# Performance work log

Measured on AMD Instinct MI355X. Metric: run time of the kernel, lower is better.

The kernel has to match this reference:

```python
import jax, jax.numpy as jnp
import numpy as np


def setup_inputs() -> dict:
    key = jax.random.key(0)
    ks = jax.random.split(key, 8)
    B, N, C, H = 4, 1024, 512, 8
    return {
        "x": jax.random.normal(ks[0], (B, N, C), jnp.float32),
        "pos": jax.random.normal(ks[1], (B, N, 3), jnp.float32),
        "w_qkv": jax.random.normal(ks[2], (C, 3 * C), jnp.float32) * 0.02,
        "b_qkv": jax.random.normal(ks[3], (3 * C,), jnp.float32) * 0.02,
        "w1": jax.random.normal(ks[4], (3, 64), jnp.float32) * 0.1,
        "b1": jax.random.normal(ks[5], (64,), jnp.float32) * 0.1,
        "w2": jax.random.normal(ks[6], (64, H), jnp.float32) * 0.1,
        "b2": jax.random.normal(ks[7], (H,), jnp.float32) * 0.1,
    }


def reference(x, pos, w_qkv, b_qkv, w1, b1, w2, b2):
    B, N, C = x.shape
    H = w2.shape[1]          # num_heads
    D = C // H               # head_dim
    scale = D ** (-0.5)

    # qkv projection -> q, k, v each [B, H, N, D]
    qkv = (x @ w_qkv + b_qkv).reshape(B, N, 3, H, D)
    qkv = jnp.transpose(qkv, (2, 0, 3, 1, 4))
    q, k, v = qkv[0], qkv[1], qkv[2]

    # pairwise unit direction vectors [B, N, N, 3]
    pos_diff = pos[:, :, None, :] - pos[:, None, :, :]
    pos_norm = jnp.linalg.norm(pos_diff, axis=-1, keepdims=True) + 1e-6
    pos_dir = pos_diff / pos_norm

    # position-MLP bias: [B, N, N, H] -> [B, H, N, N]
    h = jax.nn.relu(pos_dir @ w1 + b1)
    bias = jnp.transpose(h @ w2 + b2, (0, 3, 1, 2))

    attn = jnp.einsum("bhnd,bhmd->bhnm", q, k) * scale + bias
    attn = jax.nn.softmax(attn, axis=-1)
    out = jnp.einsum("bhnm,bhmd->bhnd", attn, v)
    return jnp.transpose(out, (0, 2, 1, 3)).reshape(B, N, C)
```

## Files before the change

kernel.cpp:

```cpp
#include <hip/hip_runtime.h>
#include <hip/hip_bf16.h>
#include <hip/hip_fp16.h>
#include <math.h>


typedef __attribute__((ext_vector_type(8))) short bh8;
typedef __attribute__((ext_vector_type(4))) float f32x4;

#define LOG2E 1.44269504f

static __device__ __forceinline__ ushort f2bf(float x) {
    __hip_bfloat16 h = __float2bfloat16(x);
    return *reinterpret_cast<ushort*>(&h);
}
static __device__ __forceinline__ float bf2f(ushort u) {
    unsigned v = ((unsigned)u) << 16;
    return __builtin_bit_cast(float, v);
}
static __device__ __forceinline__ ushort f2h(float x) {
    __half h = __float2half(x);
    return *reinterpret_cast<ushort*>(&h);
}
static __device__ __forceinline__ float h2f(ushort u) {
    __half h = __builtin_bit_cast(__half, u);
    return __half2float(h);
}

__global__ __launch_bounds__(256) void prep_kernel(
    const float* __restrict__ x, const float* __restrict__ pos,
    const float* __restrict__ w1, const float* __restrict__ wqkv,
    ushort* __restrict__ xh, ushort* __restrict__ xl,
    ushort* __restrict__ wTh, ushort* __restrict__ wTl,
    float* __restrict__ apos)
{
    __shared__ float t[64][65];
    const int bid = blockIdx.x;
    const int tid = threadIdx.x;

    if (bid < 2048) {
        const int idx = bid * 256 + tid;
        const float4 v = *(const float4*)&x[(size_t)idx * 4];
        ushort h0 = f2bf(v.x), h1 = f2bf(v.y), h2 = f2bf(v.z), h3 = f2bf(v.w);
        ushort l0 = f2bf(v.x - bf2f(h0)), l1 = f2bf(v.y - bf2f(h1));
        ushort l2 = f2bf(v.z - bf2f(h2)), l3 = f2bf(v.w - bf2f(h3));
        uint2 hu, lu;
        hu.x = (unsigned)h0 | ((unsigned)h1 << 16);
        hu.y = (unsigned)h2 | ((unsigned)h3 << 16);
        lu.x = (unsigned)l0 | ((unsigned)l1 << 16);
        lu.y = (unsigned)l2 | ((unsigned)l3 << 16);
        *(uint2*)&xh[(size_t)idx * 4] = hu;
        *(uint2*)&xl[(size_t)idx * 4] = lu;
    } else if (bid < 3072) {
        const int idx = (bid - 2048) * 256 + tid;
        const int bn = idx >> 6, j = idx & 63;
        const float px = pos[bn * 3 + 0];
        const float py = pos[bn * 3 + 1];
        const float pz = pos[bn * 3 + 2];
        apos[idx] = fmaf(px, w1[j], fmaf(py, w1[64 + j], pz * w1[128 + j]));
    } else {
        const int tb = bid - 3072;
        const int n0 = (tb % 24) * 64;
        const int k0 = (tb / 24) * 64;
        const int c = tid & 63, r4 = tid >> 6;
#pragma unroll
        for (int i = 0; i < 16; ++i) {
            const int r = i * 4 + r4;
            t[r][c] = wqkv[(size_t)(k0 + r) * 1536 + n0 + c];
        }
        __syncthreads();
#pragma unroll
        for (int i = 0; i < 16; ++i) {
            const int r = i * 4 + r4;
            const float v = t[c][r];
            const ushort hv = f2bf(v);
            wTh[(size_t)(n0 + r) * 512 + k0 + c] = hv;
            wTl[(size_t)(n0 + r) * 512 + k0 + c] = f2bf(v - bf2f(hv));
        }
    }
}

__global__ __launch_bounds__(256, 2) void qkv_mfma(
    const ushort* __restrict__ xh, const ushort* __restrict__ xl,
    const ushort* __restrict__ wTh, const ushort* __restrict__ wTl,
    const float* __restrict__ bqkv,
    ushort* __restrict__ qb, ushort* __restrict__ kb, ushort* __restrict__ vTb)
{
    __shared__ ushort Ah[128 * 68], Al[128 * 68], Bh[128 * 68], Bl[128 * 68];
    const int tid = threadIdx.x;
    const int m0 = blockIdx.x * 128;
    const int n0 = blockIdx.y * 128;
    const int wid = tid >> 6, lane = tid & 63;
    const int wr = wid >> 1, wc = wid & 1;
    const int lq = lane & 15, g = lane >> 4;

    f32x4 acc[4][4];
#pragma unroll
    for (int m = 0; m < 4; ++m)
#pragma unroll
        for (int n = 0; n < 4; ++n) acc[m][n] = (f32x4){0.f, 0.f, 0.f, 0.f};

    const int srow = tid >> 3;
    const int sc8 = (tid & 7) * 8;

    for (int kt = 0; kt < 8; ++kt) {
        const int kk0 = kt * 64;
        __syncthreads();
#pragma unroll
        for (int i = 0; i < 4; ++i) {
            const int row = i * 32 + srow;
            *(bh8*)&Ah[row * 68 + sc8] =
                *(const bh8*)&xh[(size_t)(m0 + row) * 512 + kk0 + sc8];
            *(bh8*)&Al[row * 68 + sc8] =
                *(const bh8*)&xl[(size_t)(m0 + row) * 512 + kk0 + sc8];
            *(bh8*)&Bh[row * 68 + sc8] =
                *(const bh8*)&wTh[(size_t)(n0 + row) * 512 + kk0 + sc8];
            *(bh8*)&Bl[row * 68 + sc8] =
                *(const bh8*)&wTl[(size_t)(n0 + row) * 512 + kk0 + sc8];
        }
        __syncthreads();
#pragma unroll
        for (int kc = 0; kc < 2; ++kc) {
            const int ko = kc * 32 + g * 8;
            bh8 afh[4], afl[4], bfh[4], bfl[4];
#pragma unroll
            for (int m = 0; m < 4; ++m) {
                afh[m] = *(const bh8*)&Ah[(wr * 64 + m * 16 + lq) * 68 + ko];
                afl[m] = *(const bh8*)&Al[(wr * 64 + m * 16 + lq) * 68 + ko];
            }
#pragma unroll
            for (int n = 0; n < 4; ++n) {
                bfh[n] = *(const bh8*)&Bh[(wc * 64 + n * 16 + lq) * 68 + ko];
                bfl[n] = *(const bh8*)&Bl[(wc * 64 + n * 16 + lq) * 68 + ko];
            }
#pragma unroll
            for (int m = 0; m < 4; ++m)
#pragma unroll
                for (int n = 0; n < 4; ++n) {
                    acc[m][n] = __builtin_amdgcn_mfma_f32_16x16x32_bf16(
                        afh[m], bfh[n], acc[m][n], 0, 0, 0);
                    acc[m][n] = __builtin_amdgcn_mfma_f32_16x16x32_bf16(
                        afh[m], bfl[n], acc[m][n], 0, 0, 0);
                    acc[m][n] = __builtin_amdgcn_mfma_f32_16x16x32_bf16(
                        afl[m], bfh[n], acc[m][n], 0, 0, 0);
                }
        }
    }

    const int s = n0 >> 9;
    const int rowB = m0 + wr * 64;
    const int b = rowB >> 10;
    const float QSCALE = 0.125f * LOG2E;
#pragma unroll
    for (int nt = 0; nt < 4; ++nt) {
        const int col = n0 + wc * 64 + nt * 16 + lq;
        const float bias_v = bqkv[col];
        const int h = (col >> 6) & 7, d = col & 63;
#pragma unroll
        for (int mt = 0; mt < 4; ++mt) {
            const int nloc = (rowB & 1023) + mt * 16 + g * 4;
            const float v0 = acc[mt][nt][0] + bias_v;
            const float v1 = acc[mt][nt][1] + bias_v;
            const float v2 = acc[mt][nt][2] + bias_v;
            const float v3 = acc[mt][nt][3] + bias_v;
            if (s == 0) {
                const size_t base = ((size_t)(b * 8 + h) * 1024 + nloc) * 64 + d;
                qb[base]       = f2bf(v0 * QSCALE);
                qb[base + 64]  = f2bf(v1 * QSCALE);
                qb[base + 128] = f2bf(v2 * QSCALE);
                qb[base + 192] = f2bf(v3 * QSCALE);
            } else if (s == 1) {
                const size_t base = ((size_t)(b * 8 + h) * 1024 + nloc) * 64 + d;
                kb[base]       = f2bf(v0);
                kb[base + 64]  = f2bf(v1);
                kb[base + 128] = f2bf(v2);
                kb[base + 192] = f2bf(v3);
            } else {
                uint2 u;
                u.x = (unsigned)f2bf(v0) | ((unsigned)f2bf(v1) << 16);
                u.y = (unsigned)f2bf(v2) | ((unsigned)f2bf(v3) << 16);
                *(uint2*)&vTb[((size_t)(b * 8 + h) * 64 + d) * 1024 + nloc] = u;
            }
        }
    }
}

__global__ __launch_bounds__(512, 4) void attn_fused(
    const ushort* __restrict__ qb, const ushort* __restrict__ kb,
    const ushort* __restrict__ vTb, const float* __restrict__ apos,
    const float* __restrict__ pos, const float* __restrict__ b1,
    const float* __restrict__ w2, const float* __restrict__ b2,
    float* __restrict__ outp0, float* __restrict__ outp1,
    float* __restrict__ ml0, float* __restrict__ ml1)
{
    const int bx = blockIdx.x;
    const int xcd = bx & 7;
    const int b = xcd >> 1;
    const int u = (bx >> 3) * 2 + (xcd & 1);
    const int nq0 = (u & 63) * 16;
    const int half = u >> 6;
    const int k0base = half * 512;

    float* __restrict__ outp = half ? outp1 : outp0;
    float* __restrict__ mlp  = half ? ml1 : ml0;

    const int tid = threadIdx.x;
    const int w = tid >> 6;
    const int lane = tid & 63;
    const int lq = lane & 15;
    const int g = lane >> 4;

    __shared__ __align__(16) float a_m_s[64][64];
    __shared__ __align__(16) float pos_k_s[64][4];
    __shared__ __align__(16) ushort bias_s[8 * 1100];
    __shared__ __align__(16) ushort p_lds[8][16][72];
    __shared__ float red_s[8][18];

    float a_n[16], b1r[16];
    {
        const float* anp = apos + (size_t)(b * 1024 + nq0 + lq) * 64;
        *(float4*)&a_n[0]  = *(const float4*)&anp[g * 8];
        *(float4*)&a_n[4]  = *(const float4*)&anp[g * 8 + 4];
        *(float4*)&a_n[8]  = *(const float4*)&anp[32 + g * 8];
        *(float4*)&a_n[12] = *(const float4*)&anp[32 + g * 8 + 4];
        *(float4*)&b1r[0]  = *(const float4*)&b1[g * 8];
        *(float4*)&b1r[4]  = *(const float4*)&b1[g * 8 + 4];
        *(float4*)&b1r[8]  = *(const float4*)&b1[32 + g * 8];
        *(float4*)&b1r[12] = *(const float4*)&b1[32 + g * 8 + 4];
    }
    const float px = pos[(size_t)(b * 1024 + nq0 + lq) * 3 + 0];
    const float py = pos[(size_t)(b * 1024 + nq0 + lq) * 3 + 1];
    const float pz = pos[(size_t)(b * 1024 + nq0 + lq) * 3 + 2];

    bh8 w2fa, w2fb;
#pragma unroll
    for (int e = 0; e < 8; ++e) {
        const int k0 = g * 8 + e, k1 = 32 + g * 8 + e;
        w2fa[e] = (short)((lq < 8) ? f2bf(w2[k0 * 8 + lq] * LOG2E) : 0);
        w2fb[e] = (short)((lq < 8) ? f2bf(w2[k1 * 8 + lq] * LOG2E) : 0);
    }
    const float b2r = (lq < 8) ? b2[lq] * LOG2E : 0.f;

    bh8 qf0, qf1;
    {
        const ushort* qp = qb + ((size_t)(b * 8 + w) * 1024 + nq0 + lq) * 64;
        qf0 = *(const bh8*)&qp[g * 8];
        qf1 = *(const bh8*)&qp[32 + g * 8];
    }

    f32x4 o[4];
#pragma unroll
    for (int dt = 0; dt < 4; ++dt) o[dt] = (f32x4){0.f, 0.f, 0.f, 0.f};
    float m_run = -INFINITY, l_run = 0.f;

#define STAGE(m0v) do { \
        const float4* _src = (const float4*)(apos + (size_t)(b * 1024 + (m0v)) * 64); \
        float4* _dst = (float4*)&a_m_s[0][0]; \
        _dst[tid] = _src[tid]; \
        _dst[tid + 512] = _src[tid + 512]; \
        if (tid < 192) pos_k_s[tid / 3][tid % 3] = \
            pos[(size_t)(b * 1024 + (m0v) + tid / 3) * 3 + tid % 3]; \
    } while (0)

    STAGE(k0base);
    __syncthreads();

    for (int t16 = 0; t16 < 8; ++t16) {
        const int m0 = k0base + t16 * 64;

#pragma unroll
        for (int kk = 0; kk < 8; ++kk) {
            const int jl = w * 8 + kk;
            const float kx = pos_k_s[jl][0];
            const float ky = pos_k_s[jl][1];
            const float kz = pos_k_s[jl][2];
            const float dx = px - kx, dy = py - ky, dz = pz - kz;
            const float inv =
                1.f / (sqrtf(fmaf(dx, dx, fmaf(dy, dy, dz * dz))) + 1e-6f);
            const float* am = &a_m_s[jl][0];
            bh8 hf0, hf1;
#pragma unroll
            for (int e = 0; e < 8; ++e) {
                const float h0 =
                    fmaxf(fmaf(a_n[e] - am[g * 8 + e], inv, b1r[e]), 0.f);
                const float h1 =
                    fmaxf(fmaf(a_n[8 + e] - am[32 + g * 8 + e], inv, b1r[8 + e]), 0.f);
                hf0[e] = (short)f2bf(h0);
                hf1[e] = (short)f2bf(h1);
            }
            f32x4 acc = (f32x4){0.f, 0.f, 0.f, 0.f};
            acc = __builtin_amdgcn_mfma_f32_16x16x32_bf16(hf0, w2fa, acc, 0, 0, 0);
            acc = __builtin_amdgcn_mfma_f32_16x16x32_bf16(hf1, w2fb, acc, 0, 0, 0);
            if (lq < 8) {
#pragma unroll
                for (int r = 0; r < 4; ++r)
                    bias_s[lq * 1100 + (g * 4 + r) * 68 + jl] = f2h(acc[r] + b2r);
            }
        }
        __syncthreads();

        if (t16 < 7) STAGE(m0 + 64);

        const ushort* kbp = kb + ((size_t)(b * 8 + w) * 1024 + m0) * 64;
        f32x4 s[4];
#pragma unroll
        for (int at = 0; at < 4; ++at) {
            const bh8 kf0 = *(const bh8*)&kbp[(at * 16 + lq) * 64 + g * 8];
            const bh8 kf1 = *(const bh8*)&kbp[(at * 16 + lq) * 64 + 32 + g * 8];
            f32x4 z = (f32x4){0.f, 0.f, 0.f, 0.f};
            z = __builtin_amdgcn_mfma_f32_16x16x32_bf16(kf0, qf0, z, 0, 0, 0);
            s[at] = __builtin_amdgcn_mfma_f32_16x16x32_bf16(kf1, qf1, z, 0, 0, 0);
        }

        float sv[16];
        float pmax = -INFINITY;
#pragma unroll
        for (int at = 0; at < 4; ++at) {
            const int bb = w * 1100 + lq * 68 + at * 16 + g * 4;
            const uint2 bu = *(const uint2*)&bias_s[bb];
            sv[at * 4 + 0] = s[at][0] + h2f((ushort)(bu.x & 0xffff));
            sv[at * 4 + 1] = s[at][1] + h2f((ushort)(bu.x >> 16));
            sv[at * 4 + 2] = s[at][2] + h2f((ushort)(bu.y & 0xffff));
            sv[at * 4 + 3] = s[at][3] + h2f((ushort)(bu.y >> 16));
#pragma unroll
            for (int r = 0; r < 4; ++r) pmax = fmaxf(pmax, sv[at * 4 + r]);
        }
        pmax = fmaxf(pmax, __shfl_xor(pmax, 16));
        pmax = fmaxf(pmax, __shfl_xor(pmax, 32));
        const float mnew = fmaxf(m_run, pmax);
        const float alpha = exp2f(m_run - mnew);
        m_run = mnew;

        float rs = 0.f;
        ushort pb[16];
#pragma unroll
        for (int i = 0; i < 16; ++i) {
            const float p = exp2f(sv[i] - mnew);
            pb[i] = f2bf(p);
            rs += p;
        }
        rs += __shfl_xor(rs, 16);
        rs += __shfl_xor(rs, 32);
        l_run = l_run * alpha + rs;

#pragma unroll
        for (int at = 0; at < 4; ++at) {
            uint2 uv;
            uv.x = (unsigned)pb[at * 4 + 0] | ((unsigned)pb[at * 4 + 1] << 16);
            uv.y = (unsigned)pb[at * 4 + 2] | ((unsigned)pb[at * 4 + 3] << 16);
            *(uint2*)&p_lds[w][lq][at * 16 + g * 4] = uv;
        }
        red_s[w][lq] = alpha;

        float ar[4];
#pragma unroll
        for (int r = 0; r < 4; ++r) ar[r] = red_s[w][g * 4 + r];
#pragma unroll
        for (int dt = 0; dt < 4; ++dt) {
            o[dt][0] *= ar[0]; o[dt][1] *= ar[1];
            o[dt][2] *= ar[2]; o[dt][3] *= ar[3];
        }

        const bh8 pa0 = *(const bh8*)&p_lds[w][lq][g * 8];
        const bh8 pa1 = *(const bh8*)&p_lds[w][lq][32 + g * 8];
        const ushort* vtp = vTb + ((size_t)(b * 8 + w) * 64) * 1024 + m0;
#pragma unroll
        for (int dt = 0; dt < 4; ++dt) {
            const bh8 vf0 = *(const bh8*)&vtp[(dt * 16 + lq) * 1024 + g * 8];
            const bh8 vf1 = *(const bh8*)&vtp[(dt * 16 + lq) * 1024 + 32 + g * 8];
            o[dt] = __builtin_amdgcn_mfma_f32_16x16x32_bf16(pa0, vf0, o[dt], 0, 0, 0);
            o[dt] = __builtin_amdgcn_mfma_f32_16x16x32_bf16(pa1, vf1, o[dt], 0, 0, 0);
        }
        __syncthreads();
    }

    if (g == 0) {
        float2 mlv;
        mlv.x = m_run;
        mlv.y = l_run;
        *(float2*)&mlp[((size_t)(b * 8 + w) * 1024 + nq0 + lq) * 2] = mlv;
    }
#pragma unroll
    for (int dt = 0; dt < 4; ++dt)
#pragma unroll
        for (int r = 0; r < 4; ++r)
            outp[(size_t)(b * 1024 + nq0 + g * 4 + r) * 512 + w * 64 + dt * 16 + lq] =
                o[dt][r];
#undef STAGE
}

__global__ __launch_bounds__(256) void combine_halves(
    const float* __restrict__ o0, const float* __restrict__ o1,
    const float* __restrict__ ml0, const float* __restrict__ ml1,
    float* __restrict__ outF)
{
    const int idx = blockIdx.x * 256 + threadIdx.x;
    const size_t c4 = (size_t)idx * 4;
    const int row = idx >> 7;
    const int coff = (idx & 127) * 4;
    const int h = coff >> 6;
    const int b = row >> 10, n = row & 1023;
    const size_t mli = ((size_t)(b * 8 + h) * 1024 + n) * 2;
    const float2 v0 = *(const float2*)&ml0[mli];
    const float2 v1 = *(const float2*)&ml1[mli];
    const float m = fmaxf(v0.x, v1.x);
    const float e0 = exp2f(v0.x - m), e1 = exp2f(v1.x - m);
    const float inv = 1.f / fmaf(v0.y, e0, v1.y * e1);
    const float4 a = *(const float4*)&o0[c4];
    const float4 bb = *(const float4*)&o1[c4];
    float4 r;
    r.x = fmaf(a.x, e0, bb.x * e1) * inv;
    r.y = fmaf(a.y, e0, bb.y * e1) * inv;
    r.z = fmaf(a.z, e0, bb.z * e1) * inv;
    r.w = fmaf(a.w, e0, bb.w * e1) * inv;
    *(float4*)&outF[c4] = r;
}

extern "C" void kernel_launch(void* const* d_in, const int* in_sizes, int n_in,
                              void* d_out, int out_size, void* d_ws, size_t ws_size,
                              hipStream_t stream) {
    const float* x    = (const float*)d_in[0];
    const float* pos  = (const float*)d_in[1];
    const float* wqkv = (const float*)d_in[2];
    const float* bqkv = (const float*)d_in[3];
    const float* w1   = (const float*)d_in[4];
    const float* b1   = (const float*)d_in[5];
    const float* w2   = (const float*)d_in[6];
    const float* b2   = (const float*)d_in[7];
    float* out = (float*)d_out;

    char* W = (char*)d_ws;
    ushort* qb    = (ushort*)W;
    ushort* kb    = (ushort*)(W + 4194304);
    ushort* vTb   = (ushort*)(W + 8388608);
    float*  apos  = (float*)(W + 12582912);
    ushort* xh    = (ushort*)(W + 13631488);
    ushort* xl    = (ushort*)(W + 17825792);
    float*  outp1 = (float*)(W + 13631488);
    ushort* wTh   = (ushort*)(W + 22020096);
    ushort* wTl   = (ushort*)(W + 23592960);
    float*  ml0   = (float*)(W + 22020096);
    float*  ml1   = (float*)(W + 22282240);
    float*  outp0 = out;

    hipLaunchKernelGGL(prep_kernel, dim3(3264), dim3(256), 0, stream,
                       x, pos, w1, wqkv, xh, xl, wTh, wTl, apos);
    hipLaunchKernelGGL(qkv_mfma, dim3(32, 12), dim3(256), 0, stream,
                       xh, xl, wTh, wTl, bqkv, qb, kb, vTb);
    hipLaunchKernelGGL(attn_fused, dim3(512), dim3(512), 0, stream,
                       qb, kb, vTb, apos, pos, b1, w2, b2,
                       outp0, outp1, ml0, ml1);
    hipLaunchKernelGGL(combine_halves, dim3(2048), dim3(256), 0, stream,
                       outp0, outp1, ml0, ml1, out);
}
```

Measured before the change: 203.3 us.

## Split attention keys three ways and drop x low-part in QKV GEMM

The attention kernel can now split the key range into three parts (6/5/5 tiles) instead of two when the workspace is large enough, launching more blocks to fill the GPU, and the combine kernel merges three partial results. The QKV projection no longer splits x into high and low bf16 parts: it keeps a single bf16 x, uses two MFMAs per tile instead of three, and switches to 128x64 tiles with a higher occupancy bound. This cuts GEMM work and prep traffic at the cost of x precision and an extra partial output to write and combine.

```diff
diff --git a/kernel.cpp b/kernel.cpp
--- a/kernel.cpp
+++ b/kernel.cpp
@@ -29,7 +29,7 @@
 __global__ __launch_bounds__(256) void prep_kernel(
     const float* __restrict__ x, const float* __restrict__ pos,
     const float* __restrict__ w1, const float* __restrict__ wqkv,
-    ushort* __restrict__ xh, ushort* __restrict__ xl,
+    ushort* __restrict__ xb,
     ushort* __restrict__ wTh, ushort* __restrict__ wTl,
     float* __restrict__ apos)
 {
@@ -40,16 +40,10 @@
     if (bid < 2048) {
         const int idx = bid * 256 + tid;
         const float4 v = *(const float4*)&x[(size_t)idx * 4];
-        ushort h0 = f2bf(v.x), h1 = f2bf(v.y), h2 = f2bf(v.z), h3 = f2bf(v.w);
-        ushort l0 = f2bf(v.x - bf2f(h0)), l1 = f2bf(v.y - bf2f(h1));
-        ushort l2 = f2bf(v.z - bf2f(h2)), l3 = f2bf(v.w - bf2f(h3));
-        uint2 hu, lu;
-        hu.x = (unsigned)h0 | ((unsigned)h1 << 16);
-        hu.y = (unsigned)h2 | ((unsigned)h3 << 16);
-        lu.x = (unsigned)l0 | ((unsigned)l1 << 16);
-        lu.y = (unsigned)l2 | ((unsigned)l3 << 16);
-        *(uint2*)&xh[(size_t)idx * 4] = hu;
-        *(uint2*)&xl[(size_t)idx * 4] = lu;
+        uint2 hu;
+        hu.x = (unsigned)f2bf(v.x) | ((unsigned)f2bf(v.y) << 16);
+        hu.y = (unsigned)f2bf(v.z) | ((unsigned)f2bf(v.w) << 16);
+        *(uint2*)&xb[(size_t)idx * 4] = hu;
     } else if (bid < 3072) {
         const int idx = (bid - 2048) * 256 + tid;
         const int bn = idx >> 6, j = idx & 63;
@@ -79,89 +73,88 @@
     }
 }
 
-__global__ __launch_bounds__(256, 2) void qkv_mfma(
-    const ushort* __restrict__ xh, const ushort* __restrict__ xl,
+__global__ __launch_bounds__(256, 3) void qkv_mfma(
+    const ushort* __restrict__ xb,
     const ushort* __restrict__ wTh, const ushort* __restrict__ wTl,
     const float* __restrict__ bqkv,
     ushort* __restrict__ qb, ushort* __restrict__ kb, ushort* __restrict__ vTb)
 {
-    __shared__ ushort Ah[128 * 68], Al[128 * 68], Bh[128 * 68], Bl[128 * 68];
+    __shared__ ushort Ab[128 * 68], Bh[64 * 68], Bl[64 * 68];
     const int tid = threadIdx.x;
     const int m0 = blockIdx.x * 128;
-    const int n0 = blockIdx.y * 128;
+    const int n0 = blockIdx.y * 64;
     const int wid = tid >> 6, lane = tid & 63;
-    const int wr = wid >> 1, wc = wid & 1;
     const int lq = lane & 15, g = lane >> 4;
 
-    f32x4 acc[4][4];
-#pragma unroll
-    for (int m = 0; m < 4; ++m)
+    f32x4 acc[2][4];
+#pragma unroll
+    for (int m = 0; m < 2; ++m)
 #pragma unroll
         for (int n = 0; n < 4; ++n) acc[m][n] = (f32x4){0.f, 0.f, 0.f, 0.f};
 
-    const int srow = tid >> 3;
-    const int sc8 = (tid & 7) * 8;
+    const int arow = tid >> 3;
+    const int ac = (tid & 7) * 8;
+    const int brow = tid >> 2;
+    const int bc = (tid & 3) * 16;
 
     for (int kt = 0; kt < 8; ++kt) {
         const int kk0 = kt * 64;
         __syncthreads();
 #pragma unroll
         for (int i = 0; i < 4; ++i) {
-            const int row = i * 32 + srow;
-            *(bh8*)&Ah[row * 68 + sc8] =
-                *(const bh8*)&xh[(size_t)(m0 + row) * 512 + kk0 + sc8];
-            *(bh8*)&Al[row * 68 + sc8] =
-                *(const bh8*)&xl[(size_t)(m0 + row) * 512 + kk0 + sc8];
-            *(bh8*)&Bh[row * 68 + sc8] =
-                *(const bh8*)&wTh[(size_t)(n0 + row) * 512 + kk0 + sc8];
-            *(bh8*)&Bl[row * 68 + sc8] =
-                *(const bh8*)&wTl[(size_t)(n0 + row) * 512 + kk0 + sc8];
-        }
+            const int row = i * 32 + arow;
+            *(bh8*)&Ab[row * 68 + ac] =
+                *(const bh8*)&xb[(size_t)(m0 + row) * 512 + kk0 + ac];
+        }
+        *(bh8*)&Bh[brow * 68 + bc] =
+            *(const bh8*)&wTh[(size_t)(n0 + brow) * 512 + kk0 + bc];
+        *(bh8*)&Bh[brow * 68 + bc + 8] =
+            *(const bh8*)&wTh[(size_t)(n0 + brow) * 512 + kk0 + bc + 8];
+        *(bh8*)&Bl[brow * 68 + bc] =
+            *(const bh8*)&wTl[(size_t)(n0 + brow) * 512 + kk0 + bc];
+        *(bh8*)&Bl[brow * 68 + bc + 8] =
+            *(const bh8*)&wTl[(size_t)(n0 + brow) * 512 + kk0 + bc + 8];
         __syncthreads();
 #pragma unroll
         for (int kc = 0; kc < 2; ++kc) {
             const int ko = kc * 32 + g * 8;
-            bh8 afh[4], afl[4], bfh[4], bfl[4];
-#pragma unroll
-            for (int m = 0; m < 4; ++m) {
-                afh[m] = *(const bh8*)&Ah[(wr * 64 + m * 16 + lq) * 68 + ko];
-                afl[m] = *(const bh8*)&Al[(wr * 64 + m * 16 + lq) * 68 + ko];
+            bh8 af[2], bfh[4], bfl[4];
+#pragma unroll
+            for (int m = 0; m < 2; ++m)
+                af[m] = *(const bh8*)&Ab[(wid * 32 + m * 16 + lq) * 68 + ko];
+#pragma unroll
+            for (int n = 0; n < 4; ++n) {
+                bfh[n] = *(const bh8*)&Bh[(n * 16 + lq) * 68 + ko];
+                bfl[n] = *(const bh8*)&Bl[(n * 16 + lq) * 68 + ko];
             }
 #pragma unroll
-            for (int n = 0; n < 4; ++n) {
-                bfh[n] = *(const bh8*)&Bh[(wc * 64 + n * 16 + lq) * 68 + ko];
-                bfl[n] = *(const bh8*)&Bl[(wc * 64 + n * 16 + lq) * 68 + ko];
-            }
-#pragma unroll
-            for (int m = 0; m < 4; ++m)
+            for (int m = 0; m < 2; ++m)
 #pragma unroll
                 for (int n = 0; n < 4; ++n) {
                     acc[m][n] = __builtin_amdgcn_mfma_f32_16x16x32_bf16(
-                        afh[m], bfh[n], acc[m][n], 0, 0, 0);
+                        af[m], bfh[n], acc[m][n], 0, 0, 0);
                     acc[m][n] = __builtin_amdgcn_mfma_f32_16x16x32_bf16(
-                        afh[m], bfl[n], acc[m][n], 0, 0, 0);
-                    acc[m][n] = __builtin_amdgcn_mfma_f32_16x16x32_bf16(
-                        afl[m], bfh[n], acc[m][n], 0, 0, 0);
+                        af[m], bfl[n], acc[m][n], 0, 0, 0);
                 }
         }
     }
 
     const int s = n0 >> 9;
-    const int rowB = m0 + wr * 64;
-    const int b = rowB >> 10;
+    const int h = (n0 >> 6) & 7;
     const float QSCALE = 0.125f * LOG2E;
 #pragma unroll
-    for (int nt = 0; nt < 4; ++nt) {
-        const int col = n0 + wc * 64 + nt * 16 + lq;
+    for (int ntf = 0; ntf < 4; ++ntf) {
+        const int col = n0 + ntf * 16 + lq;
         const float bias_v = bqkv[col];
-        const int h = (col >> 6) & 7, d = col & 63;
-#pragma unroll
-        for (int mt = 0; mt < 4; ++mt) {
-            const int nloc = (rowB & 1023) + mt * 16 + g * 4;
-            const float v0 = acc[mt][nt][0] + bias_v;
-            const float v1 = acc[mt][nt][1] + bias_v;
-            const float v2 = acc[mt][nt][2] + bias_v;
-            const float v3 = acc[mt][nt][3] + bias_v;
+        const int d = col & 63;
+#pragma unroll
+        for (int mf = 0; mf < 2; ++mf) {
+            const int row = m0 + wid * 32 + mf * 16 + g * 4;
+            const int b = row >> 10, nloc = row & 1023;
+            const float v0 = acc[mf][ntf][0] + bias_v;
+            const float v1 = acc[mf][ntf][1] + bias_v;
+            const float v2 = acc[mf][ntf][2] + bias_v;
+            const float v3 = acc[mf][ntf][3] + bias_v;
             if (s == 0) {
                 const size_t base = ((size_t)(b * 8 + h) * 1024 + nloc) * 64 + d;
                 qb[base]       = f2bf(v0 * QSCALE);
@@ -190,18 +183,22 @@
     const float* __restrict__ pos, const float* __restrict__ b1,
     const float* __restrict__ w2, const float* __restrict__ b2,
     float* __restrict__ outp0, float* __restrict__ outp1,
-    float* __restrict__ ml0, float* __restrict__ ml1)
+    float* __restrict__ outp2,
+    float* __restrict__ ml0, float* __restrict__ ml1,
+    float* __restrict__ ml2, int nparts)
 {
     const int bx = blockIdx.x;
     const int xcd = bx & 7;
     const int b = xcd >> 1;
     const int u = (bx >> 3) * 2 + (xcd & 1);
     const int nq0 = (u & 63) * 16;
-    const int half = u >> 6;
-    const int k0base = half * 512;
-
-    float* __restrict__ outp = half ? outp1 : outp0;
-    float* __restrict__ mlp  = half ? ml1 : ml0;
+    const int part = u >> 6;
+    int k0, nt;
+    if (nparts == 2) { k0 = part * 512; nt = 8; }
+    else { k0 = (part == 0) ? 0 : (part == 1 ? 384 : 704); nt = (part == 0) ? 6 : 5; }
+
+    float* __restrict__ outp = (part == 0) ? outp0 : (part == 1 ? outp1 : outp2);
+    float* __restrict__ mlp  = (part == 0) ? ml0 : (part == 1 ? ml1 : ml2);
 
     const int tid = threadIdx.x;
     const int w = tid >> 6;
@@ -234,9 +231,9 @@
     bh8 w2fa, w2fb;
 #pragma unroll
     for (int e = 0; e < 8; ++e) {
-        const int k0 = g * 8 + e, k1 = 32 + g * 8 + e;
-        w2fa[e] = (short)((lq < 8) ? f2bf(w2[k0 * 8 + lq] * LOG2E) : 0);
-        w2fb[e] = (short)((lq < 8) ? f2bf(w2[k1 * 8 + lq] * LOG2E) : 0);
+        const int k0e = g * 8 + e, k1e = 32 + g * 8 + e;
+        w2fa[e] = (short)((lq < 8) ? f2bf(w2[k0e * 8 + lq] * LOG2E) : 0);
+        w2fb[e] = (short)((lq < 8) ? f2bf(w2[k1e * 8 + lq] * LOG2E) : 0);
     }
     const float b2r = (lq < 8) ? b2[lq] * LOG2E : 0.f;
 
@@ -261,11 +258,11 @@
             pos[(size_t)(b * 1024 + (m0v) + tid / 3) * 3 + tid % 3]; \
     } while (0)
 
-    STAGE(k0base);
+    STAGE(k0);
     __syncthreads();
 
-    for (int t16 = 0; t16 < 8; ++t16) {
-        const int m0 = k0base + t16 * 64;
+    for (int t16 = 0; t16 < nt; ++t16) {
+        const int m0 = k0 + t16 * 64;
 
 #pragma unroll
         for (int kk = 0; kk < 8; ++kk) {
@@ -298,7 +295,7 @@
         }
         __syncthreads();
 
-        if (t16 < 7) STAGE(m0 + 64);
+        if (t16 < nt - 1) STAGE(m0 + 64);
 
         const ushort* kbp = kb + ((size_t)(b * 8 + w) * 1024 + m0) * 64;
         f32x4 s[4];
@@ -388,10 +385,11 @@
 #undef STAGE
 }
 
-__global__ __launch_bounds__(256) void combine_halves(
-    const float* __restrict__ o0, const float* __restrict__ o1,
+__global__ __launch_bounds__(256) void combine_parts(
+    const float* __restrict__ o1, const float* __restrict__ o2,
     const float* __restrict__ ml0, const float* __restrict__ ml1,
-    float* __restrict__ outF)
+    const float* __restrict__ ml2,
+    float* __restrict__ outF, int nparts)
 {
     const int idx = blockIdx.x * 256 + threadIdx.x;
     const size_t c4 = (size_t)idx * 4;
@@ -402,16 +400,21 @@
     const size_t mli = ((size_t)(b * 8 + h) * 1024 + n) * 2;
     const float2 v0 = *(const float2*)&ml0[mli];
     const float2 v1 = *(const float2*)&ml1[mli];
-    const float m = fmaxf(v0.x, v1.x);
+    float2 v2 = make_float2(-INFINITY, 0.f);
+    if (nparts == 3) v2 = *(const float2*)&ml2[mli];
+    const float m = fmaxf(fmaxf(v0.x, v1.x), v2.x);
     const float e0 = exp2f(v0.x - m), e1 = exp2f(v1.x - m);
-    const float inv = 1.f / fmaf(v0.y, e0, v1.y * e1);
-    const float4 a = *(const float4*)&o0[c4];
+    const float e2 = (nparts == 3) ? exp2f(v2.x - m) : 0.f;
+    const float inv = 1.f / (v0.y * e0 + v1.y * e1 + v2.y * e2);
+    const float4 a = *(const float4*)&outF[c4];
     const float4 bb = *(const float4*)&o1[c4];
+    float4 cc = make_float4(0.f, 0.f, 0.f, 0.f);
+    if (nparts == 3) cc = *(const float4*)&o2[c4];
     float4 r;
-    r.x = fmaf(a.x, e0, bb.x * e1) * inv;
-    r.y = fmaf(a.y, e0, bb.y * e1) * inv;
-    r.z = fmaf(a.z, e0, bb.z * e1) * inv;
-    r.w = fmaf(a.w, e0, bb.w * e1) * inv;
+    r.x = (a.x * e0 + bb.x * e1 + cc.x * e2) * inv;
+    r.y = (a.y * e0 + bb.y * e1 + cc.y * e2) * inv;
+    r.z = (a.z * e0 + bb.z * e1 + cc.z * e2) * inv;
+    r.w = (a.w * e0 + bb.w * e1 + cc.w * e2) * inv;
     *(float4*)&outF[c4] = r;
 }
 
@@ -429,26 +432,43 @@
     float* out = (float*)d_out;
 
     char* W = (char*)d_ws;
-    ushort* qb    = (ushort*)W;
-    ushort* kb    = (ushort*)(W + 4194304);
-    ushort* vTb   = (ushort*)(W + 8388608);
-    float*  apos  = (float*)(W + 12582912);
-    ushort* xh    = (ushort*)(W + 13631488);
-    ushort* xl    = (ushort*)(W + 17825792);
-    float*  outp1 = (float*)(W + 13631488);
-    ushort* wTh   = (ushort*)(W + 22020096);
-    ushort* wTl   = (ushort*)(W + 23592960);
-    float*  ml0   = (float*)(W + 22020096);
-    float*  ml1   = (float*)(W + 22282240);
-    float*  outp0 = out;
+    ushort* qb   = (ushort*)W;
+    ushort* kb   = (ushort*)(W + 4194304);
+    ushort* vTb  = (ushort*)(W + 8388608);
+    float*  apos = (float*)(W + 12582912);
+    ushort* xb   = (ushort*)(W + 13631488);
+
+    const size_t NEED3 = 31195136;
+    const int nparts = (ws_size >= NEED3) ? 3 : 2;
+
+    ushort *wTh, *wTl;
+    float *outp1, *outp2, *ml0, *ml1, *ml2;
+    if (nparts == 3) {
+        wTh   = (ushort*)(W + 17825792);
+        wTl   = (ushort*)(W + 19398656);
+        outp1 = (float*)(W + 13631488);
+        outp2 = (float*)(W + 22020096);
+        ml0   = (float*)(W + 30408704);
+        ml1   = (float*)(W + 30670848);
+        ml2   = (float*)(W + 30932992);
+    } else {
+        wTh   = (ushort*)(W + 22020096);
+        wTl   = (ushort*)(W + 23592960);
+        outp1 = (float*)(W + 13631488);
+        outp2 = outp1;
+        ml0   = (float*)(W + 22020096);
+        ml1   = (float*)(W + 22282240);
+        ml2   = ml0;
+    }
+    float* outp0 = out;
 
     hipLaunchKernelGGL(prep_kernel, dim3(3264), dim3(256), 0, stream,
-                       x, pos, w1, wqkv, xh, xl, wTh, wTl, apos);
-    hipLaunchKernelGGL(qkv_mfma, dim3(32, 12), dim3(256), 0, stream,
-                       xh, xl, wTh, wTl, bqkv, qb, kb, vTb);
-    hipLaunchKernelGGL(attn_fused, dim3(512), dim3(512), 0, stream,
+                       x, pos, w1, wqkv, xb, wTh, wTl, apos);
+    hipLaunchKernelGGL(qkv_mfma, dim3(32, 24), dim3(256), 0, stream,
+                       xb, wTh, wTl, bqkv, qb, kb, vTb);
+    hipLaunchKernelGGL(attn_fused, dim3(256 * nparts), dim3(512), 0, stream,
                        qb, kb, vTb, apos, pos, b1, w2, b2,
-                       outp0, outp1, ml0, ml1);
-    hipLaunchKernelGGL(combine_halves, dim3(2048), dim3(256), 0, stream,
-                       outp0, outp1, ml0, ml1, out);
-}
+                       outp0, outp1, outp2, ml0, ml1, ml2, nparts);
+    hipLaunchKernelGGL(combine_parts, dim3(2048), dim3(256), 0, stream,
+                       outp1, outp2, ml0, ml1, ml2, out, nparts);
+}
```

After: 206.0 us. No clear change (+1.3%).
